# Kernel optimization log

Measured on AMD Instinct MI355X. Metric: run time of the kernel, lower is better.

The kernel has to match this reference:

```python
import jax, jax.numpy as jnp
import numpy as np

B, C_IN, H, W = 8, 64, 32, 32
DK, DV, NH, KS = 64, 64, 4, 3
DKH = DK // NH
DVH = DV // NH


def conv2d(x, w, b, stride=1, padding=1):
    out = jax.lax.conv_general_dilated(
        x, w, (stride, stride), [(padding, padding), (padding, padding)],
        dimension_numbers=('NCHW', 'OIHW', 'NCHW'))
    return out + b[None, :, None, None]


def rel_to_abs(x):
    # x: (B, Nh, L, 2L-1) -> (B, Nh, L, L) via skewing trick
    b, nh, L, _ = x.shape
    x = jnp.pad(x, ((0, 0), (0, 0), (0, 0), (0, 1)))          # (B,Nh,L,2L)
    flat = x.reshape(b, nh, L * 2 * L)
    flat = jnp.pad(flat, ((0, 0), (0, 0), (0, L - 1)))
    final = flat.reshape(b, nh, L + 1, 2 * L - 1)
    return final[:, :, :L, L - 1:]


def relative_logits_1d(q, rel_k, h, w, nh, case):
    # q: (B, Nh, h, w, d); rel_k: (2w-1, d)
    b = q.shape[0]
    rel = jnp.einsum('bhxyd,md->bhxym', q, rel_k)             # (B,Nh,h,w,2w-1)
    rel = rel.reshape(b, nh * h, w, 2 * w - 1)
    rel = rel_to_abs(rel)                                     # (B,Nh*h,w,w)
    rel = rel.reshape(b, nh, h, w, w)
    rel = jnp.broadcast_to(rel[:, :, :, None], (b, nh, h, h, w, w))
    if case == 'w':
        rel = jnp.swapaxes(rel, 3, 4)
    else:  # 'h'
        rel = jnp.swapaxes(rel, 2, 4)
        rel = jnp.swapaxes(rel, 4, 5)
        rel = jnp.swapaxes(rel, 3, 5)
    return rel.reshape(b, nh, h * w, h * w)


def relative_logits(q, rel_w, rel_h):
    # q: (B, Nh, dkh, H, W) (already scaled)
    qt = jnp.transpose(q, (0, 1, 3, 4, 2))                    # (B,Nh,H,W,d)
    w_logits = relative_logits_1d(qt, rel_w, H, W, NH, 'w')
    h_logits = relative_logits_1d(jnp.swapaxes(qt, 2, 3), rel_h, W, H, NH, 'h')
    return h_logits, w_logits


def compute_qkv(x, w, b):
    qkv = conv2d(x, w, b)
    n, _, h, ww = qkv.shape
    q, k, v = jnp.split(qkv, [DK, 2 * DK], axis=1)
    q = q.reshape(n, NH, DKH, h, ww) * (DKH ** -0.5)
    k = k.reshape(n, NH, DKH, h, ww)
    v = v.reshape(n, NH, DVH, h, ww)
    return q, k, v


def setup_inputs() -> dict:
    key = jax.random.key(0)
    ks = jax.random.split(key, 16)
    cqkv = 2 * DK + DV
    s = 0.05
    return {
        'x1': jax.random.normal(ks[0], (B, C_IN, H, W), jnp.float32),
        'x2': jax.random.normal(ks[1], (B, C_IN, H, W), jnp.float32),
        'x12': jax.random.normal(ks[2], (B, C_IN, H, W), jnp.float32),
        'w_qkv1': jax.random.normal(ks[3], (cqkv, C_IN, KS, KS), jnp.float32) * s,
        'b_qkv1': jax.random.normal(ks[4], (cqkv,), jnp.float32) * s,
        'w_qkv2': jax.random.normal(ks[5], (cqkv, C_IN, KS, KS), jnp.float32) * s,
        'b_qkv2': jax.random.normal(ks[6], (cqkv,), jnp.float32) * s,
        'w_qkv12': jax.random.normal(ks[7], (cqkv, C_IN, KS, KS), jnp.float32) * s,
        'b_qkv12': jax.random.normal(ks[8], (cqkv,), jnp.float32) * s,
        'w_out': jax.random.normal(ks[9], (DV, DV, 1, 1), jnp.float32) * s,
        'b_out': jax.random.normal(ks[10], (DV,), jnp.float32) * s,
        'rel_w': jax.random.normal(ks[11], (2 * W - 1, DKH), jnp.float32),
        'rel_h': jax.random.normal(ks[12], (2 * H - 1, DKH), jnp.float32),
    }


def _forward(x1, x2, x12, w_qkv1, b_qkv1, w_qkv2, b_qkv2, w_qkv12, b_qkv12,
             w_out, b_out, rel_w, rel_h):
    q1, k1, v1 = compute_qkv(x1, w_qkv1, b_qkv1)
    q2, k2, v2 = compute_qkv(x2, w_qkv2, b_qkv2)
    q12, k12, v12 = compute_qkv(x12, w_qkv12, b_qkv12)
    hw = H * W
    fq1 = q1.reshape(B, NH, DKH, hw)
    fq2 = q2.reshape(B, NH, DKH, hw)
    fq12 = q12.reshape(B, NH, DKH, hw)
    fk1 = k1.reshape(B, NH, DKH, hw)
    fk2 = k2.reshape(B, NH, DKH, hw)
    fk12 = k12.reshape(B, NH, DKH, hw)
    fv1 = v1.reshape(B, NH, DVH, hw)
    fv2 = v2.reshape(B, NH, DVH, hw)
    fv12 = v12.reshape(B, NH, DVH, hw)

    logits1 = jnp.einsum('bhdi,bhdj->bhij', fq1, fk12)
    logits2 = jnp.einsum('bhdi,bhdj->bhij', fq2, fk12)
    logits12 = (jnp.einsum('bhdi,bhdj->bhij', fq12, fk1)
                - jnp.einsum('bhdi,bhdj->bhij', fq12, fk2))
    h_rel, w_rel = relative_logits(q1, rel_w, rel_h)
    logits1 = logits1 + h_rel + w_rel

    w1 = jax.nn.softmax(logits1, axis=-1)
    w2 = jax.nn.softmax(logits2, axis=-1)
    w12 = jax.nn.softmax(logits12, axis=-1)

    def attend(weights, fv):
        o = jnp.einsum('bhij,bhdj->bhid', weights, fv)        # (B,Nh,HW,dvh)
        o = o.reshape(B, NH, DVH, H, W)                        # raw reshape (as in torch)
        o = o.reshape(B, NH * DVH, H, W)
        return conv2d(o, w_out, b_out, padding=0)              # attn_out1 used for all (faithful)

    return attend(w1, fv1), attend(w2, fv2), attend(w12, fv12)


def reference(x1, x2, x12, w_qkv1, b_qkv1, w_qkv2, b_qkv2, w_qkv12, b_qkv12,
              w_out, b_out, rel_w, rel_h):
    return _forward(x1, x2, x12, w_qkv1, b_qkv1, w_qkv2, b_qkv2,
                    w_qkv12, b_qkv12, w_out, b_out, rel_w, rel_h)
```

## Files before the change

### kernel.cpp

```cpp
#include <hip/hip_runtime.h>
#include <math.h>

#define Bn 8
#define CIN 64
#define HH 32
#define WW 32
#define HW 1024
#define CQKV 192
#define NHh 4
#define DKHd 16
#define DVHd 16
#define QSCALE 0.36067376f

typedef _Float16 half4_t __attribute__((ext_vector_type(4)));
typedef _Float16 half8_t __attribute__((ext_vector_type(8)));
typedef __fp16 fp16x2_t __attribute__((ext_vector_type(2)));
typedef __fp16 fp16x4_t __attribute__((ext_vector_type(4)));
typedef float f32x4 __attribute__((ext_vector_type(4)));

#if __has_builtin(__builtin_amdgcn_exp2f)
#define EXP2F(x) __builtin_amdgcn_exp2f(x)
#else
#define EXP2F(x) exp2f(x)
#endif

static __device__ __forceinline__ half4_t pack4(float a, float b, float c, float d)
{
#if __has_builtin(__builtin_amdgcn_cvt_pkrtz)
    fp16x2_t lo = __builtin_amdgcn_cvt_pkrtz(a, b);
    fp16x2_t hi = __builtin_amdgcn_cvt_pkrtz(c, d);
    fp16x4_t v4 = __builtin_shufflevector(lo, hi, 0, 1, 2, 3);
    return __builtin_bit_cast(half4_t, v4);
#else
    half4_t r;
    r[0] = (_Float16)a; r[1] = (_Float16)b; r[2] = (_Float16)c; r[3] = (_Float16)d;
    return r;
#endif
}

__global__ __launch_bounds__(256) void prep_wf_kernel(
    const float* __restrict__ w1, const float* __restrict__ w2,
    const float* __restrict__ w12, _Float16* __restrict__ wf)
{
    const int f = blockIdx.x * 256 + threadIdx.x;
    if (f >= 3 * 12 * 36 * 64) return;
    const int lane = f & 63;
    int r = f >> 6;
    const int ks = r % 36; r /= 36;
    const int ct = r % 12; const int s = r / 12;
    const float* w = (s == 0) ? w1 : (s == 1) ? w2 : w12;

    const int tap = ks >> 2;
    const int ci_b = (ks & 3) * 16 + (lane >> 4) * 4;
    const int co = ct * 16 + (lane & 15);
    const float scale = (co < 64) ? QSCALE : 1.f;

    half4_t v;
    #pragma unroll
    for (int j = 0; j < 4; ++j)
        v[j] = (_Float16)(w[((size_t)co * 64 + ci_b + j) * 9 + tap] * scale);
    *reinterpret_cast<half4_t*>(&wf[(size_t)f * 4]) = v;
}

__global__ __launch_bounds__(256) void conv_mfma_kernel(
    const float* __restrict__ x1, const float* __restrict__ x2,
    const float* __restrict__ x12, const _Float16* __restrict__ wf,
    const float* __restrict__ b1, const float* __restrict__ b2,
    const float* __restrict__ b12, _Float16* __restrict__ qkv)
{
    __shared__ _Float16 xs[8704];
    const int strip = blockIdx.x;
    const int b = blockIdx.y, s = blockIdx.z;
    const int sb = s * Bn + b;
    const int tid = threadIdx.x;
    const int w = tid >> 6, lane = tid & 63, g = lane >> 4, lq = lane & 15;
    const int y0 = strip * 2;

    {
        const float* xsrc = (s == 0) ? x1 : (s == 1) ? x2 : x12;
        const float* xb = xsrc + (size_t)b * CIN * HW;
        const int ci = tid & 63;
        const int ry = tid >> 6;
        const int gy = y0 - 1 + ry;
        f32x4 rowv[8];
        if ((unsigned)gy < 32u) {
            const f32x4* rp = reinterpret_cast<const f32x4*>(
                &xb[(size_t)ci * HW + gy * 32]);
            #pragma unroll
            for (int u = 0; u < 8; ++u) rowv[u] = rp[u];
        } else {
            #pragma unroll
            for (int u = 0; u < 8; ++u) rowv[u] = (f32x4){0.f, 0.f, 0.f, 0.f};
        }
        const int cchunk = ci >> 2, cbase = ci & 3;
        #pragma unroll
        for (int xx = 0; xx < 34; ++xx) {
            const int gx = xx - 1;
            float v = 0.f;
            if ((unsigned)gx < 32u) v = rowv[gx >> 2][gx & 3];
            xs[(ry * 34 + xx) * 64 + (((cchunk ^ (xx & 15)) << 2) + cbase)] =
                (_Float16)v;
        }
    }
    __syncthreads();

    f32x4 acc[3][4];
    #pragma unroll
    for (int cc = 0; cc < 3; ++cc)
        #pragma unroll
        for (int t = 0; t < 4; ++t) acc[cc][t] = (f32x4){0.f, 0.f, 0.f, 0.f};

    const _Float16* wfs = wf + ((size_t)(s * 12 + w * 3) * 36) * 256;

    #pragma unroll
    for (int tap = 0; tap < 9; ++tap) {
        const int ky = tap / 3, kx = tap % 3;
        #pragma unroll
        for (int sub = 0; sub < 4; ++sub) {
            const int ks = tap * 4 + sub;
            half4_t af[3];
            #pragma unroll
            for (int cc = 0; cc < 3; ++cc)
                af[cc] = *reinterpret_cast<const half4_t*>(
                    &wfs[((size_t)cc * 36 + ks) * 256 + lane * 4]);
            half4_t bf[4];
            #pragma unroll
            for (int t = 0; t < 4; ++t) {
                const int ry = (t >> 1) + ky;
                const int xx = (t & 1) * 16 + lq + kx;
                const int cichunk = sub * 4 + g;
                bf[t] = *reinterpret_cast<const half4_t*>(
                    &xs[(ry * 34 + xx) * 64 + ((cichunk ^ (xx & 15)) << 2)]);
            }
            #pragma unroll
            for (int cc = 0; cc < 3; ++cc)
                #pragma unroll
                for (int t = 0; t < 4; ++t)
                    acc[cc][t] = __builtin_amdgcn_mfma_f32_16x16x16f16(
                        af[cc], bf[t], acc[cc][t], 0, 0, 0);
        }
    }

    const float* bi = (s == 0) ? b1 : (s == 1) ? b2 : b12;
    _Float16* outb = qkv + (size_t)sb * CQKV * HW;
    #pragma unroll
    for (int cc = 0; cc < 3; ++cc) {
        const int ct = w * 3 + cc;
        const float bsc = (ct < 4) ? QSCALE : 1.f;
        const f32x4 bv4 = *reinterpret_cast<const f32x4*>(&bi[ct * 16 + g * 4]);
        #pragma unroll
        for (int t = 0; t < 4; ++t) {
            const int px = strip * 64 + t * 16 + lq;
            #pragma unroll
            for (int r = 0; r < 4; ++r) {
                const int ch = ct * 16 + g * 4 + r;
                outb[(size_t)ch * HW + px] = (_Float16)(acc[cc][t][r] + bsc * bv4[r]);
            }
        }
    }
}

__global__ __launch_bounds__(256) void qrel_kernel(
    const _Float16* __restrict__ qkv,
    const float* __restrict__ relw, const float* __restrict__ relh,
    _Float16* __restrict__ qrel_t)
{
    __shared__ float rw_s[63 * 16], rh_s[63 * 16];
    const int bh = blockIdx.y;
    const int b  = bh >> 2, h = bh & 3;
    const int i  = blockIdx.x * 256 + threadIdx.x;

    for (int e = threadIdx.x; e < 1008; e += 256) {
        rw_s[e] = relw[e];
        rh_s[e] = relh[e];
    }
    __syncthreads();

    const _Float16* qb = qkv + ((size_t)b * CQKV + h * 16) * HW + i;
    f32x4 qv[4];
    #pragma unroll
    for (int d = 0; d < 16; ++d) qv[d >> 2][d & 3] = (float)qb[(size_t)d * HW];

    const int x1 = i & 31, y1 = i >> 5;
    _Float16 row[64];
    #pragma unroll
    for (int c = 0; c < 32; ++c) {
        const f32x4* wp = reinterpret_cast<const f32x4*>(&rw_s[(c + 31 - x1) * 16]);
        const f32x4* hp = reinterpret_cast<const f32x4*>(&rh_s[(c + 31 - y1) * 16]);
        float sw = 0.f, sh = 0.f;
        #pragma unroll
        for (int dq = 0; dq < 4; ++dq) {
            const f32x4 wv = wp[dq], hv = hp[dq], qq = qv[dq];
            #pragma unroll
            for (int e = 0; e < 4; ++e) {
                sw = fmaf(qq[e], wv[e], sw);
                sh = fmaf(qq[e], hv[e], sh);
            }
        }
        row[c]      = (_Float16)sw;
        row[32 + c] = (_Float16)sh;
    }

    _Float16* dst = qrel_t + ((size_t)bh * HW + i) * 64;
    #pragma unroll
    for (int u = 0; u < 8; ++u)
        *reinterpret_cast<half8_t*>(&dst[u * 8]) =
            *reinterpret_cast<const half8_t*>(&row[u * 8]);
}

__global__ __launch_bounds__(512, 4) void attn_mfma_kernel(
    const _Float16* __restrict__ qkv,
    const _Float16* __restrict__ qrel_t,
    _Float16* __restrict__ o16)
{
    __shared__ _Float16 kf_lds[16384];
    __shared__ _Float16 vf_lds[16384];

    const int bid = blockIdx.x;
    const int S    = bid % 3;
    const int rest = bid / 3;
    const int bh   = rest & 31;
    const int qb   = rest >> 5;
    const int b   = bh >> 2, hd = bh & 3;
    const int tid = threadIdx.x;
    const int w    = tid >> 6;
    const int lane = tid & 63;
    const int g    = lane >> 4;
    const int lq   = lane & 15;
    const size_t SS = (size_t)Bn * CQKV * HW;

    const _Float16* qsrc = qkv + S * SS + ((size_t)b * CQKV + hd * 16) * HW;
    const _Float16* vsrc = qkv + S * SS + ((size_t)b * CQKV + 128 + hd * 16) * HW;
    const _Float16* k1p;
    const _Float16* k2p;
    if (S == 2) {
        k1p = qkv + 0 * SS + ((size_t)b * CQKV + 64 + hd * 16) * HW;
        k2p = qkv + 1 * SS + ((size_t)b * CQKV + 64 + hd * 16) * HW;
    } else {
        k1p = qkv + 2 * SS + ((size_t)b * CQKV + 64 + hd * 16) * HW;
        k2p = k1p;
    }

    #pragma unroll 4
    for (int it = 0; it < 8; ++it) {
        const int idx = it * 512 + tid;
        const int kt  = idx >> 6, l = idx & 63;
        const int row = l & 15;
        const int d0  = (l >> 4) * 4;
        const int lofs = (kt >> 1) * 512 + l * 8 + (kt & 1) * 4;

        const int key = kt * 16 + row;
        half4_t kh;
        if (S == 2) {
            #pragma unroll
            for (int j = 0; j < 4; ++j)
                kh[j] = (_Float16)((float)k1p[(size_t)(d0 + j) * HW + key]
                                 - (float)k2p[(size_t)(d0 + j) * HW + key]);
        } else {
            #pragma unroll
            for (int j = 0; j < 4; ++j)
                kh[j] = k1p[(size_t)(d0 + j) * HW + key];
        }
        *reinterpret_cast<half4_t*>(&kf_lds[lofs]) = kh;

        *reinterpret_cast<half4_t*>(&vf_lds[lofs]) =
            *reinterpret_cast<const half4_t*>(&vsrc[(size_t)row * HW + kt * 16 + d0]);
    }

    const int qb0 = qb * 128 + w * 16;
    const int i   = qb0 + lq;

    half4_t qf;
    #pragma unroll
    for (int j = 0; j < 4; ++j) qf[j] = qsrc[(size_t)(g * 4 + j) * HW + i];

    f32x4 crw0 = {0.f, 0.f, 0.f, 0.f}, crw1 = {0.f, 0.f, 0.f, 0.f};
    half8_t qhr[4];
    if (S == 0) {
        const _Float16* rrow = qrel_t + ((size_t)bh * HW + i) * 64;
        const half4_t rw0 = *reinterpret_cast<const half4_t*>(&rrow[g * 4]);
        const half4_t rw1 = *reinterpret_cast<const half4_t*>(&rrow[16 + g * 4]);
        #pragma unroll
        for (int r = 0; r < 4; ++r) {
            crw0[r] = (float)rw0[r];
            crw1[r] = (float)rw1[r];
        }
        #pragma unroll
        for (int u = 0; u < 4; ++u)
            qhr[u] = *reinterpret_cast<const half8_t*>(&rrow[32 + u * 8]);
    } else {
        #pragma unroll
        for (int u = 0; u < 4; ++u)
            qhr[u] = (half8_t)(_Float16)0.f;
    }

    __syncthreads();

    f32x4 acc  = {0.f, 0.f, 0.f, 0.f};
    f32x4 accS = {0.f, 0.f, 0.f, 0.f};
    float m = -1e30f;
    const half4_t onef = {(_Float16)1.f, (_Float16)1.f, (_Float16)1.f, (_Float16)1.f};

    #pragma unroll
    for (int c = 0; c < 32; c += 2) {
        const half8_t kk0 = *reinterpret_cast<const half8_t*>(&kf_lds[c * 512 + lane * 8]);
        const half8_t kk1 = *reinterpret_cast<const half8_t*>(&kf_lds[(c + 1) * 512 + lane * 8]);
        const half8_t vv0 = *reinterpret_cast<const half8_t*>(&vf_lds[c * 512 + lane * 8]);
        const half8_t vv1 = *reinterpret_cast<const half8_t*>(&vf_lds[(c + 1) * 512 + lane * 8]);

        const float rh0 = (float)qhr[c >> 3][c & 7];
        const float rh1 = (float)qhr[(c + 1) >> 3][(c + 1) & 7];

        f32x4 s0 = __builtin_amdgcn_mfma_f32_16x16x16f16(
            __builtin_shufflevector(kk0, kk0, 0, 1, 2, 3), qf, crw0, 0, 0, 0);
        f32x4 s1 = __builtin_amdgcn_mfma_f32_16x16x16f16(
            __builtin_shufflevector(kk0, kk0, 4, 5, 6, 7), qf, crw1, 0, 0, 0);
        f32x4 s2 = __builtin_amdgcn_mfma_f32_16x16x16f16(
            __builtin_shufflevector(kk1, kk1, 0, 1, 2, 3), qf, crw0, 0, 0, 0);
        f32x4 s3 = __builtin_amdgcn_mfma_f32_16x16x16f16(
            __builtin_shufflevector(kk1, kk1, 4, 5, 6, 7), qf, crw1, 0, 0, 0);

        float a0 = fmaxf(fmaxf(s0[0], s0[1]), fmaxf(s0[2], s0[3]));
        float a1 = fmaxf(fmaxf(s1[0], s1[1]), fmaxf(s1[2], s1[3]));
        float a2 = fmaxf(fmaxf(s2[0], s2[1]), fmaxf(s2[2], s2[3]));
        float a3 = fmaxf(fmaxf(s3[0], s3[1]), fmaxf(s3[2], s3[3]));
        const float vmax = fmaxf(fmaxf(a0, a1) + rh0, fmaxf(a2, a3) + rh1);

        if (!__all(vmax <= m + 11.53f)) {
            float wmax = fmaxf(vmax, __shfl_xor(vmax, 16));
            wmax = fmaxf(wmax, __shfl_xor(wmax, 32));
            const float mnew = fmaxf(m, wmax);
            const float fsc  = EXP2F(m - mnew);
            m = mnew;
            acc  *= fsc;
            accS *= fsc;
        }

        const float mm0 = m - rh0;
        const float mm1 = m - rh1;

        const half4_t pa = pack4(EXP2F(s0[0] - mm0), EXP2F(s0[1] - mm0),
                                 EXP2F(s0[2] - mm0), EXP2F(s0[3] - mm0));
        const half4_t pb = pack4(EXP2F(s1[0] - mm0), EXP2F(s1[1] - mm0),
                                 EXP2F(s1[2] - mm0), EXP2F(s1[3] - mm0));
        const half4_t pc = pack4(EXP2F(s2[0] - mm1), EXP2F(s2[1] - mm1),
                                 EXP2F(s2[2] - mm1), EXP2F(s2[3] - mm1));
        const half4_t pd = pack4(EXP2F(s3[0] - mm1), EXP2F(s3[1] - mm1),
                                 EXP2F(s3[2] - mm1), EXP2F(s3[3] - mm1));

        acc = __builtin_amdgcn_mfma_f32_16x16x16f16(
            __builtin_shufflevector(vv0, vv0, 0, 1, 2, 3), pa, acc, 0, 0, 0);
        acc = __builtin_amdgcn_mfma_f32_16x16x16f16(
            __builtin_shufflevector(vv0, vv0, 4, 5, 6, 7), pb, acc, 0, 0, 0);
        acc = __builtin_amdgcn_mfma_f32_16x16x16f16(
            __builtin_shufflevector(vv1, vv1, 0, 1, 2, 3), pc, acc, 0, 0, 0);
        acc = __builtin_amdgcn_mfma_f32_16x16x16f16(
            __builtin_shufflevector(vv1, vv1, 4, 5, 6, 7), pd, acc, 0, 0, 0);

        accS = __builtin_amdgcn_mfma_f32_16x16x16f16(onef, pa, accS, 0, 0, 0);
        accS = __builtin_amdgcn_mfma_f32_16x16x16f16(onef, pb, accS, 0, 0, 0);
        accS = __builtin_amdgcn_mfma_f32_16x16x16f16(onef, pc, accS, 0, 0, 0);
        accS = __builtin_amdgcn_mfma_f32_16x16x16f16(onef, pd, accS, 0, 0, 0);
    }

    const float inv = 1.f / accS[0];

    _Float16* op = o16 + (size_t)(S * Bn + b) * 65536 + (size_t)hd * 16384
                 + (size_t)i * 16 + g * 4;
    *reinterpret_cast<half4_t*>(op) =
        pack4(acc[0] * inv, acc[1] * inv, acc[2] * inv, acc[3] * inv);
}

__global__ __launch_bounds__(256) void out_conv_mfma_kernel(
    const _Float16* __restrict__ o16, const float* __restrict__ wout,
    const float* __restrict__ bout, float* __restrict__ out)
{
    __shared__ _Float16 wls[4096];
    __shared__ _Float16 ols[4096];
    const int strip = blockIdx.x;
    const int sb    = blockIdx.y;
    const int tid = threadIdx.x;
    const int w = tid >> 6, lane = tid & 63, g = lane >> 4, lq = lane & 15;

    {
        const int row = tid >> 2;
        const int cg  = (tid & 3) * 4;
        #pragma unroll
        for (int k = 0; k < 4; ++k) {
            const int c = cg + k;
            const f32x4 wv = *reinterpret_cast<const f32x4*>(&wout[(row * 16 + c) * 4]);
            *reinterpret_cast<half4_t*>(&wls[row * 64 + ((c ^ (row & 15)) << 2)]) =
                pack4(wv[0], wv[1], wv[2], wv[3]);
        }
    }
    {
        const _Float16* osrc = o16 + (size_t)sb * 65536 + strip * 64;
        #pragma unroll
        for (int it = 0; it < 2; ++it) {
            const int idx = it * 256 + tid;
            const int c   = idx >> 3;
            const int t0  = (idx & 7) * 8;
            const half8_t v = *reinterpret_cast<const half8_t*>(
                &osrc[(size_t)c * HW + t0]);
            #pragma unroll
            for (int e = 0; e < 8; ++e) {
                const int t = t0 + e;
                ols[t * 64 + ((((c >> 2) ^ (t & 15)) << 2) + (c & 3))] = v[e];
            }
        }
    }
    __syncthreads();

    half4_t af[4];
    #pragma unroll
    for (int ks = 0; ks < 4; ++ks)
        af[ks] = *reinterpret_cast<const half4_t*>(
            &wls[(w * 16 + lq) * 64 + (((ks * 4 + g) ^ lq) << 2)]);

    const f32x4 bv4 = *reinterpret_cast<const f32x4*>(&bout[w * 16 + g * 4]);

    #pragma unroll
    for (int pt = 0; pt < 4; ++pt) {
        f32x4 acc = {0.f, 0.f, 0.f, 0.f};
        #pragma unroll
        for (int ks = 0; ks < 4; ++ks) {
            const half4_t bf = *reinterpret_cast<const half4_t*>(
                &ols[(pt * 16 + lq) * 64 + (((ks * 4 + g) ^ lq) << 2)]);
            acc = __builtin_amdgcn_mfma_f32_16x16x16f16(af[ks], bf, acc, 0, 0, 0);
        }
        const int px = strip * 64 + pt * 16 + lq;
        #pragma unroll
        for (int r = 0; r < 4; ++r) {
            const int co = w * 16 + g * 4 + r;
            out[((size_t)sb * 64 + co) * HW + px] = acc[r] + bv4[r];
        }
    }
}

extern "C" void kernel_launch(void* const* d_in, const int* in_sizes, int n_in,
                              void* d_out, int out_size, void* d_ws, size_t ws_size,
                              hipStream_t stream)
{
    const float* x1   = (const float*)d_in[0];
    const float* x2   = (const float*)d_in[1];
    const float* x12  = (const float*)d_in[2];
    const float* wq1  = (const float*)d_in[3];
    const float* bq1  = (const float*)d_in[4];
    const float* wq2  = (const float*)d_in[5];
    const float* bq2  = (const float*)d_in[6];
    const float* wq12 = (const float*)d_in[7];
    const float* bq12 = (const float*)d_in[8];
    const float* wout = (const float*)d_in[9];
    const float* bout = (const float*)d_in[10];
    const float* relw = (const float*)d_in[11];
    const float* relh = (const float*)d_in[12];

    _Float16* qkv16  = (_Float16*)d_ws;
    _Float16* o16    = qkv16 + (size_t)4718592;
    _Float16* qrel_t = o16 + (size_t)1572864;
    _Float16* wf     = qrel_t + (size_t)2097152;

    prep_wf_kernel<<<dim3(324), 256, 0, stream>>>(wq1, wq2, wq12, wf);

    conv_mfma_kernel<<<dim3(16, 8, 3), 256, 0, stream>>>(
        x1, x2, x12, wf, bq1, bq2, bq12, qkv16);

    qrel_kernel<<<dim3(4, 32), 256, 0, stream>>>(qkv16, relw, relh, qrel_t);

    attn_mfma_kernel<<<dim3(768), 512, 0, stream>>>(qkv16, qrel_t, o16);

    out_conv_mfma_kernel<<<dim3(16, 24), 256, 0, stream>>>(
        o16, wout, bout, (float*)d_out);
}
```

Measured before the change: 72.59 us.

## Split attention keys into two halves with a separate softmax combine kernel

The attention kernel now gives each block half of the keys (split-K flash-decoding style), which doubles the grid and halves the LDS per block so more blocks can be resident. Each half writes unnormalized fp32 accumulators plus its running max and sum. A new combine kernel merges the two halves with log-sum-exp rescaling and writes the fp16 output. This adds a kernel launch and extra global traffic for the partial results, and each block now pays the K/V staging and setup cost for half the work.

```diff
diff --git a/kernel.cpp b/kernel.cpp
--- a/kernel.cpp
+++ b/kernel.cpp
@@ -208,19 +208,21 @@
             *reinterpret_cast<const half8_t*>(&row[u * 8]);
 }
 
-__global__ __launch_bounds__(512, 4) void attn_mfma_kernel(
+__global__ __launch_bounds__(512, 8) void attn_mfma_kernel(
     const _Float16* __restrict__ qkv,
     const _Float16* __restrict__ qrel_t,
-    _Float16* __restrict__ o16)
-{
-    __shared__ _Float16 kf_lds[16384];
-    __shared__ _Float16 vf_lds[16384];
+    float* __restrict__ pacc, float2* __restrict__ pms)
+{
+    __shared__ _Float16 kf_lds[8192];
+    __shared__ _Float16 vf_lds[8192];
 
     const int bid = blockIdx.x;
-    const int S    = bid % 3;
-    const int rest = bid / 3;
-    const int bh   = rest & 31;
-    const int qb   = rest >> 5;
+    const int kh   = bid & 1;
+    const int r2   = bid >> 1;
+    const int S    = r2 % 3;
+    const int r3   = r2 / 3;
+    const int bh   = r3 & 31;
+    const int qb   = r3 >> 5;
     const int b   = bh >> 2, hd = bh & 3;
     const int tid = threadIdx.x;
     const int w    = tid >> 6;
@@ -242,29 +244,29 @@
     }
 
     #pragma unroll 4
-    for (int it = 0; it < 8; ++it) {
+    for (int it = 0; it < 4; ++it) {
         const int idx = it * 512 + tid;
-        const int kt  = idx >> 6, l = idx & 63;
+        const int ktl = idx >> 6, l = idx & 63;
         const int row = l & 15;
         const int d0  = (l >> 4) * 4;
-        const int lofs = (kt >> 1) * 512 + l * 8 + (kt & 1) * 4;
-
-        const int key = kt * 16 + row;
-        half4_t kh;
+        const int lofs = (ktl >> 1) * 512 + l * 8 + (ktl & 1) * 4;
+
+        const int key = kh * 512 + ktl * 16 + row;
+        half4_t kh4;
         if (S == 2) {
             #pragma unroll
             for (int j = 0; j < 4; ++j)
-                kh[j] = (_Float16)((float)k1p[(size_t)(d0 + j) * HW + key]
-                                 - (float)k2p[(size_t)(d0 + j) * HW + key]);
+                kh4[j] = (_Float16)((float)k1p[(size_t)(d0 + j) * HW + key]
+                                  - (float)k2p[(size_t)(d0 + j) * HW + key]);
         } else {
             #pragma unroll
             for (int j = 0; j < 4; ++j)
-                kh[j] = k1p[(size_t)(d0 + j) * HW + key];
-        }
-        *reinterpret_cast<half4_t*>(&kf_lds[lofs]) = kh;
+                kh4[j] = k1p[(size_t)(d0 + j) * HW + key];
+        }
+        *reinterpret_cast<half4_t*>(&kf_lds[lofs]) = kh4;
 
         *reinterpret_cast<half4_t*>(&vf_lds[lofs]) =
-            *reinterpret_cast<const half4_t*>(&vsrc[(size_t)row * HW + kt * 16 + d0]);
+            *reinterpret_cast<const half4_t*>(&vsrc[(size_t)row * HW + kh * 512 + ktl * 16 + d0]);
     }
 
     const int qb0 = qb * 128 + w * 16;
@@ -275,7 +277,7 @@
     for (int j = 0; j < 4; ++j) qf[j] = qsrc[(size_t)(g * 4 + j) * HW + i];
 
     f32x4 crw0 = {0.f, 0.f, 0.f, 0.f}, crw1 = {0.f, 0.f, 0.f, 0.f};
-    half8_t qhr[4];
+    half8_t qhr[2];
     if (S == 0) {
         const _Float16* rrow = qrel_t + ((size_t)bh * HW + i) * 64;
         const half4_t rw0 = *reinterpret_cast<const half4_t*>(&rrow[g * 4]);
@@ -285,13 +287,11 @@
             crw0[r] = (float)rw0[r];
             crw1[r] = (float)rw1[r];
         }
-        #pragma unroll
-        for (int u = 0; u < 4; ++u)
-            qhr[u] = *reinterpret_cast<const half8_t*>(&rrow[32 + u * 8]);
+        qhr[0] = *reinterpret_cast<const half8_t*>(&rrow[32 + kh * 16]);
+        qhr[1] = *reinterpret_cast<const half8_t*>(&rrow[40 + kh * 16]);
     } else {
-        #pragma unroll
-        for (int u = 0; u < 4; ++u)
-            qhr[u] = (half8_t)(_Float16)0.f;
+        qhr[0] = (half8_t)(_Float16)0.f;
+        qhr[1] = (half8_t)(_Float16)0.f;
     }
 
     __syncthreads();
@@ -302,7 +302,7 @@
     const half4_t onef = {(_Float16)1.f, (_Float16)1.f, (_Float16)1.f, (_Float16)1.f};
 
     #pragma unroll
-    for (int c = 0; c < 32; c += 2) {
+    for (int c = 0; c < 16; c += 2) {
         const half8_t kk0 = *reinterpret_cast<const half8_t*>(&kf_lds[c * 512 + lane * 8]);
         const half8_t kk1 = *reinterpret_cast<const half8_t*>(&kf_lds[(c + 1) * 512 + lane * 8]);
         const half8_t vv0 = *reinterpret_cast<const half8_t*>(&vf_lds[c * 512 + lane * 8]);
@@ -363,12 +363,34 @@
         accS = __builtin_amdgcn_mfma_f32_16x16x16f16(onef, pd, accS, 0, 0, 0);
     }
 
-    const float inv = 1.f / accS[0];
-
-    _Float16* op = o16 + (size_t)(S * Bn + b) * 65536 + (size_t)hd * 16384
-                 + (size_t)i * 16 + g * 4;
-    *reinterpret_cast<half4_t*>(op) =
-        pack4(acc[0] * inv, acc[1] * inv, acc[2] * inv, acc[3] * inv);
+    const int qh = (S * Bn + b) * NHh + hd;
+    float* pa = pacc + (size_t)kh * 1572864 + ((size_t)qh * 1024 + i) * 16 + g * 4;
+    *reinterpret_cast<f32x4*>(pa) = acc;
+    if (g == 0)
+        pms[(size_t)kh * 98304 + (size_t)qh * 1024 + i] = make_float2(m, accS[0]);
+}
+
+__global__ __launch_bounds__(256) void combine_kernel(
+    const float* __restrict__ pacc, const float2* __restrict__ pms,
+    _Float16* __restrict__ o16)
+{
+    const int idx = blockIdx.x * 256 + threadIdx.x;
+    const int g = idx & 3;
+    const int q = idx >> 2;
+
+    const float2 ms0 = pms[q];
+    const float2 ms1 = pms[98304 + q];
+    const f32x4 a0 = *reinterpret_cast<const f32x4*>(&pacc[(size_t)q * 16 + g * 4]);
+    const f32x4 a1 = *reinterpret_cast<const f32x4*>(&pacc[(size_t)1572864 + (size_t)q * 16 + g * 4]);
+
+    const float M  = fmaxf(ms0.x, ms1.x);
+    const float w0 = EXP2F(ms0.x - M);
+    const float w1 = EXP2F(ms1.x - M);
+    const float inv = 1.f / (w0 * ms0.y + w1 * ms1.y);
+
+    *reinterpret_cast<half4_t*>(&o16[(size_t)q * 16 + g * 4]) =
+        pack4((w0 * a0[0] + w1 * a1[0]) * inv, (w0 * a0[1] + w1 * a1[1]) * inv,
+              (w0 * a0[2] + w1 * a1[2]) * inv, (w0 * a0[3] + w1 * a1[3]) * inv);
 }
 
 __global__ __launch_bounds__(256) void out_conv_mfma_kernel(
@@ -459,6 +481,8 @@
     _Float16* o16    = qkv16 + (size_t)4718592;
     _Float16* qrel_t = o16 + (size_t)1572864;
     _Float16* wf     = qrel_t + (size_t)2097152;
+    float*    pacc   = (float*)(wf + (size_t)331776);
+    float2*   pms    = (float2*)(pacc + (size_t)3145728);
 
     prep_wf_kernel<<<dim3(324), 256, 0, stream>>>(wq1, wq2, wq12, wf);
 
@@ -467,7 +491,9 @@
 
     qrel_kernel<<<dim3(4, 32), 256, 0, stream>>>(qkv16, relw, relh, qrel_t);
 
-    attn_mfma_kernel<<<dim3(768), 512, 0, stream>>>(qkv16, qrel_t, o16);
+    attn_mfma_kernel<<<dim3(1536), 512, 0, stream>>>(qkv16, qrel_t, pacc, pms);
+
+    combine_kernel<<<dim3(1536), 256, 0, stream>>>(pacc, pms, o16);
 
     out_conv_mfma_kernel<<<dim3(16, 24), 256, 0, stream>>>(
         o16, wout, bout, (float*)d_out);
```

After: 71.87 us. No clear change (-1.0%).

## Split attention key range across two wave groups and merge softmax partials in LDS

Applied to the files above, without the earlier changes.

The attention kernel now launches 1024 threads per block: two groups of eight waves each process half of the keys for the same 128 queries. Each half keeps its own running max, sum and output accumulator, and the second half passes its partials through shared memory so the first can rescale and combine them. This shortens the serial per-wave loop and adds more waves for latency hiding. The cost is an extra LDS exchange, a block-wide barrier and lower blocks per CU from the larger block and higher LDS use.

```diff
diff --git a/kernel.cpp b/kernel.cpp
--- a/kernel.cpp
+++ b/kernel.cpp
@@ -208,13 +208,15 @@
             *reinterpret_cast<const half8_t*>(&row[u * 8]);
 }
 
-__global__ __launch_bounds__(512, 4) void attn_mfma_kernel(
+__global__ __launch_bounds__(1024, 2) void attn_mfma_kernel(
     const _Float16* __restrict__ qkv,
     const _Float16* __restrict__ qrel_t,
     _Float16* __restrict__ o16)
 {
     __shared__ _Float16 kf_lds[16384];
     __shared__ _Float16 vf_lds[16384];
+    __shared__ float    macc[2048];
+    __shared__ float2   mms[128];
 
     const int bid = blockIdx.x;
     const int S    = bid % 3;
@@ -224,6 +226,8 @@
     const int b   = bh >> 2, hd = bh & 3;
     const int tid = threadIdx.x;
     const int w    = tid >> 6;
+    const int kh   = w >> 3;
+    const int wq   = w & 7;
     const int lane = tid & 63;
     const int g    = lane >> 4;
     const int lq   = lane & 15;
@@ -241,41 +245,40 @@
         k2p = k1p;
     }
 
-    #pragma unroll 4
-    for (int it = 0; it < 8; ++it) {
-        const int idx = it * 512 + tid;
+    #pragma unroll
+    for (int it = 0; it < 4; ++it) {
+        const int idx = it * 1024 + tid;
         const int kt  = idx >> 6, l = idx & 63;
         const int row = l & 15;
         const int d0  = (l >> 4) * 4;
         const int lofs = (kt >> 1) * 512 + l * 8 + (kt & 1) * 4;
 
         const int key = kt * 16 + row;
-        half4_t kh;
+        half4_t kh4;
         if (S == 2) {
             #pragma unroll
             for (int j = 0; j < 4; ++j)
-                kh[j] = (_Float16)((float)k1p[(size_t)(d0 + j) * HW + key]
-                                 - (float)k2p[(size_t)(d0 + j) * HW + key]);
+                kh4[j] = (_Float16)((float)k1p[(size_t)(d0 + j) * HW + key]
+                                  - (float)k2p[(size_t)(d0 + j) * HW + key]);
         } else {
             #pragma unroll
             for (int j = 0; j < 4; ++j)
-                kh[j] = k1p[(size_t)(d0 + j) * HW + key];
-        }
-        *reinterpret_cast<half4_t*>(&kf_lds[lofs]) = kh;
+                kh4[j] = k1p[(size_t)(d0 + j) * HW + key];
+        }
+        *reinterpret_cast<half4_t*>(&kf_lds[lofs]) = kh4;
 
         *reinterpret_cast<half4_t*>(&vf_lds[lofs]) =
             *reinterpret_cast<const half4_t*>(&vsrc[(size_t)row * HW + kt * 16 + d0]);
     }
 
-    const int qb0 = qb * 128 + w * 16;
-    const int i   = qb0 + lq;
+    const int i = qb * 128 + wq * 16 + lq;
 
     half4_t qf;
     #pragma unroll
     for (int j = 0; j < 4; ++j) qf[j] = qsrc[(size_t)(g * 4 + j) * HW + i];
 
     f32x4 crw0 = {0.f, 0.f, 0.f, 0.f}, crw1 = {0.f, 0.f, 0.f, 0.f};
-    half8_t qhr[4];
+    half8_t qhr[2];
     if (S == 0) {
         const _Float16* rrow = qrel_t + ((size_t)bh * HW + i) * 64;
         const half4_t rw0 = *reinterpret_cast<const half4_t*>(&rrow[g * 4]);
@@ -285,13 +288,11 @@
             crw0[r] = (float)rw0[r];
             crw1[r] = (float)rw1[r];
         }
-        #pragma unroll
-        for (int u = 0; u < 4; ++u)
-            qhr[u] = *reinterpret_cast<const half8_t*>(&rrow[32 + u * 8]);
+        qhr[0] = *reinterpret_cast<const half8_t*>(&rrow[32 + kh * 16]);
+        qhr[1] = *reinterpret_cast<const half8_t*>(&rrow[40 + kh * 16]);
     } else {
-        #pragma unroll
-        for (int u = 0; u < 4; ++u)
-            qhr[u] = (half8_t)(_Float16)0.f;
+        qhr[0] = (half8_t)(_Float16)0.f;
+        qhr[1] = (half8_t)(_Float16)0.f;
     }
 
     __syncthreads();
@@ -300,13 +301,14 @@
     f32x4 accS = {0.f, 0.f, 0.f, 0.f};
     float m = -1e30f;
     const half4_t onef = {(_Float16)1.f, (_Float16)1.f, (_Float16)1.f, (_Float16)1.f};
-
-    #pragma unroll
-    for (int c = 0; c < 32; c += 2) {
-        const half8_t kk0 = *reinterpret_cast<const half8_t*>(&kf_lds[c * 512 + lane * 8]);
-        const half8_t kk1 = *reinterpret_cast<const half8_t*>(&kf_lds[(c + 1) * 512 + lane * 8]);
-        const half8_t vv0 = *reinterpret_cast<const half8_t*>(&vf_lds[c * 512 + lane * 8]);
-        const half8_t vv1 = *reinterpret_cast<const half8_t*>(&vf_lds[(c + 1) * 512 + lane * 8]);
+    const int kbase = kh * 8192;
+
+    #pragma unroll
+    for (int c = 0; c < 16; c += 2) {
+        const half8_t kk0 = *reinterpret_cast<const half8_t*>(&kf_lds[kbase + c * 512 + lane * 8]);
+        const half8_t kk1 = *reinterpret_cast<const half8_t*>(&kf_lds[kbase + (c + 1) * 512 + lane * 8]);
+        const half8_t vv0 = *reinterpret_cast<const half8_t*>(&vf_lds[kbase + c * 512 + lane * 8]);
+        const half8_t vv1 = *reinterpret_cast<const half8_t*>(&vf_lds[kbase + (c + 1) * 512 + lane * 8]);
 
         const float rh0 = (float)qhr[c >> 3][c & 7];
         const float rh1 = (float)qhr[(c + 1) >> 3][(c + 1) & 7];
@@ -363,12 +365,26 @@
         accS = __builtin_amdgcn_mfma_f32_16x16x16f16(onef, pd, accS, 0, 0, 0);
     }
 
-    const float inv = 1.f / accS[0];
-
-    _Float16* op = o16 + (size_t)(S * Bn + b) * 65536 + (size_t)hd * 16384
-                 + (size_t)i * 16 + g * 4;
-    *reinterpret_cast<half4_t*>(op) =
-        pack4(acc[0] * inv, acc[1] * inv, acc[2] * inv, acc[3] * inv);
+    const int qloc = wq * 16 + lq;
+    if (kh == 1) {
+        *reinterpret_cast<f32x4*>(&macc[qloc * 16 + g * 4]) = acc;
+        if (g == 0) mms[qloc] = make_float2(m, accS[0]);
+    }
+    __syncthreads();
+    if (kh == 0) {
+        const f32x4 a1 = *reinterpret_cast<const f32x4*>(&macc[qloc * 16 + g * 4]);
+        const float2 ms1 = mms[qloc];
+        const float M  = fmaxf(m, ms1.x);
+        const float w0 = EXP2F(m - M);
+        const float w1 = EXP2F(ms1.x - M);
+        const float inv = 1.f / (w0 * accS[0] + w1 * ms1.y);
+
+        _Float16* op = o16 + (size_t)(S * Bn + b) * 65536 + (size_t)hd * 16384
+                     + (size_t)i * 16 + g * 4;
+        *reinterpret_cast<half4_t*>(op) =
+            pack4((w0 * acc[0] + w1 * a1[0]) * inv, (w0 * acc[1] + w1 * a1[1]) * inv,
+                  (w0 * acc[2] + w1 * a1[2]) * inv, (w0 * acc[3] + w1 * a1[3]) * inv);
+    }
 }
 
 __global__ __launch_bounds__(256) void out_conv_mfma_kernel(
@@ -467,7 +483,7 @@
 
     qrel_kernel<<<dim3(4, 32), 256, 0, stream>>>(qkv16, relw, relh, qrel_t);
 
-    attn_mfma_kernel<<<dim3(768), 512, 0, stream>>>(qkv16, qrel_t, o16);
+    attn_mfma_kernel<<<dim3(768), 1024, 0, stream>>>(qkv16, qrel_t, o16);
 
     out_conv_mfma_kernel<<<dim3(16, 24), 256, 0, stream>>>(
         o16, wout, bout, (float*)d_out);
```

New measurement: 77.50 us. 1.07x slower.
